# Performance work log

Measured on AMD Instinct MI355X. Metric: run time of the kernel, lower is better.

The kernel has to match this reference:

```python
import jax, jax.numpy as jnp
import numpy as np

V = 16384      # total nodes
G = 32         # nodes per graph (512 graphs)
D = 256        # node embedding dim == hidden_size
N = 8          # heads
H = 32         # head size
I = 1024       # intermediate size
LN_EPS = 1e-12


def _layer_norm(x, g, b):
    mu = jnp.mean(x, axis=-1, keepdims=True)
    var = jnp.mean(jnp.square(x - mu), axis=-1, keepdims=True)
    return (x - mu) * jax.lax.rsqrt(var + LN_EPS) * g + b


def setup_inputs() -> dict:
    key = jax.random.key(0)
    ks = jax.random.split(key, 5)
    node_embeddings = jax.random.normal(ks[0], (V, D), jnp.float32)
    # fully-connected pairs within each graph of size G (sorted by source node)
    idx = np.arange(V, dtype=np.int32).reshape(-1, G)          # [num_graphs, G]
    src = np.repeat(idx, G, axis=1).reshape(-1)                # [P]
    dst = np.tile(idx, (1, G)).reshape(-1)                     # [P]
    in_graph_node_pairs = jnp.asarray(np.stack([src, dst], axis=-1))  # [P, 2]
    s = 0.02
    return {
        "node_embeddings": node_embeddings,
        "in_graph_node_pairs": in_graph_node_pairs,
        "W_qkv": jax.random.normal(ks[1], (D, 3 * N * H), jnp.float32) * s,
        "W_o": jax.random.normal(ks[2], (N * H, D), jnp.float32) * s,
        "ln1_g": jnp.ones((D,), jnp.float32),
        "ln1_b": jnp.zeros((D,), jnp.float32),
        "W_i": jax.random.normal(ks[3], (D, I), jnp.float32) * s,
        "W_out2": jax.random.normal(ks[4], (I, D), jnp.float32) * s,
        "ln2_g": jnp.ones((D,), jnp.float32),
        "ln2_b": jnp.zeros((D,), jnp.float32),
    }


def reference(node_embeddings, in_graph_node_pairs, W_qkv, W_o, ln1_g, ln1_b,
              W_i, W_out2, ln2_g, ln2_b):
    nV = node_embeddings.shape[0]
    src = in_graph_node_pairs[:, 0]
    dst = in_graph_node_pairs[:, 1]
    # QKV projection -> [V, N, 3H] -> split
    qkv = (node_embeddings @ W_qkv).reshape(nV, N, 3 * H)
    q, k, v = jnp.split(qkv, 3, axis=-1)                       # each [V, N, H]
    # per-pair scores [P, N]
    scores = jnp.einsum('phi,phi->ph', q[src], k[dst]) / jnp.sqrt(jnp.float32(H))
    # segment softmax over source node, all heads at once
    m = jax.ops.segment_max(scores, src, num_segments=nV)       # [V, N]
    e = jnp.exp(scores - m[src])
    denom = jax.ops.segment_sum(e, src, num_segments=nV)        # [V, N]
    w = e / denom[src]                                          # [P, N]
    # weighted value scatter-sum -> [V, N, H]
    wv = w[:, :, None] * v[dst]
    att = jax.ops.segment_sum(wv, src, num_segments=nV).reshape(nV, N * H)
    # output projection + residual + LN
    pre = _layer_norm(att @ W_o + node_embeddings, ln1_g, ln1_b)
    inter = jax.nn.gelu(pre @ W_i, approximate=False)
    out = _layer_norm(inter @ W_out2 + pre, ln2_g, ln2_b)
    return out
```

## Files before the change

### kernel.cpp

```cpp
#include <hip/hip_runtime.h>
#include <math.h>

#define V 16384
#define D 256
#define NH 256
#define THREE_NH 768
#define IDIM 1024
#define LN_EPS 1e-12f
#define SCL 0.17677669529663687f

typedef short s16x8 __attribute__((ext_vector_type(8)));
typedef float f32x4 __attribute__((ext_vector_type(4)));

__device__ inline unsigned short f2bf(float f) {
    unsigned u = __float_as_uint(f);
    u += 0x7fffu + ((u >> 16) & 1u);
    return (unsigned short)(u >> 16);
}
__device__ inline float bf2f(unsigned short s) {
    return __uint_as_float(((unsigned)s) << 16);
}

__device__ inline float fast_erf(float x) {
    float ax = fabsf(x);
    float t  = 1.f / fmaf(0.3275911f, ax, 1.f);
    float p  = fmaf(fmaf(fmaf(fmaf(1.061405429f, t, -1.453152027f), t,
                              1.421413741f), t, -0.284496736f), t, 0.254829592f);
    float e  = 1.f - p * t * __expf(-ax * ax);
    return copysignf(e, x);
}

__device__ inline void gl2lds16(const unsigned short* g, unsigned short* l) {
    __builtin_amdgcn_global_load_lds(
        (__attribute__((address_space(1))) void*)(g),
        (__attribute__((address_space(3))) void*)(l), 16, 0, 0);
}

template <int ROWS_T>
__device__ inline void stage(const unsigned short* __restrict__ src, size_t row0,
                             int ldk, int k0, unsigned short* lds, int wv, int lane) {
    constexpr int PER_WAVE = ROWS_T / 32;
    #pragma unroll
    for (int i = 0; i < PER_WAVE; ++i) {
        const int seg = wv * PER_WAVE + i;
        const int r = seg * 8 + (lane >> 3);
        const int c = (lane & 7) ^ (r & 7);
        gl2lds16(src + (row0 + (size_t)r) * ldk + k0 + c * 8, lds + seg * 512);
    }
}

__device__ inline s16x8 fragld(const unsigned short* lds, int row, int chunk) {
    return *(const s16x8*)&lds[row * 64 + ((chunk ^ (row & 7)) << 3)];
}

__global__ __launch_bounds__(256) void prep(const float* __restrict__ X,
                                            unsigned short* __restrict__ Xb,
                                            const float* __restrict__ Wqkv,
                                            const float* __restrict__ Wo,
                                            const float* __restrict__ Wi,
                                            const float* __restrict__ Wo2,
                                            unsigned short* __restrict__ WqkvT,
                                            unsigned short* __restrict__ WoT,
                                            unsigned short* __restrict__ WiT,
                                            unsigned short* __restrict__ Wo2T) {
    const int b = blockIdx.x, t = threadIdx.x;
    if (b >= 768) {
        int i = (b - 768) * 256 + t;
        float4 v = ((const float4*)X)[i];
        ushort4 o;
        o.x = f2bf(v.x); o.y = f2bf(v.y); o.z = f2bf(v.z); o.w = f2bf(v.w);
        ((ushort4*)Xb)[i] = o;
        return;
    }
    __shared__ float tile[32][33];
    const float* W; unsigned short* Wt; int K, N, bx, by;
    if (b < 192)      { W = Wqkv; Wt = WqkvT; K = 256;  N = 768;  bx = b & 7;          by = b >> 3; }
    else if (b < 256) { W = Wo;   Wt = WoT;   K = 256;  N = 256;  bx = (b - 192) & 7;  by = (b - 192) >> 3; }
    else if (b < 512) { W = Wi;   Wt = WiT;   K = 256;  N = 1024; bx = (b - 256) & 7;  by = (b - 256) >> 3; }
    else              { W = Wo2;  Wt = Wo2T;  K = 1024; N = 256;  bx = (b - 512) & 31; by = (b - 512) >> 5; }
    const int k0 = bx * 32, n0 = by * 32;
    #pragma unroll
    for (int p = 0; p < 4; ++p) {
        int idx = t + p * 256, r = idx >> 5, c = idx & 31;
        tile[r][c] = W[(size_t)(k0 + r) * N + n0 + c];
    }
    __syncthreads();
    #pragma unroll
    for (int p = 0; p < 4; ++p) {
        int idx = t + p * 256, r = idx >> 5, c = idx & 31;
        Wt[(size_t)(n0 + r) * K + k0 + c] = f2bf(tile[c][r]);
    }
}

template <int K, int N, int EPI>
__global__ __launch_bounds__(256) void gemm128(const unsigned short* __restrict__ A,
                                               const unsigned short* __restrict__ Bt,
                                               unsigned short* __restrict__ C) {
    __shared__ unsigned short As[128 * 64];
    __shared__ unsigned short Bs[128 * 64];
    constexpr int NCOL = N / 128;
    const int b = blockIdx.x;
    const int idx = b >> 3;
    const int r0 = ((b & 7) * 16 + idx / NCOL) * 128;
    const int c0 = (idx % NCOL) * 128;
    const int t = threadIdx.x;
    const int wv = t >> 6, lane = t & 63, q = lane >> 4, l16 = lane & 15;
    const int wr = (wv >> 1) * 64, wc = (wv & 1) * 64;
    f32x4 acc[4][4] = {};

    for (int k0 = 0; k0 < K; k0 += 64) {
        __syncthreads();
        stage<128>(A,  (size_t)r0, K, k0, As, wv, lane);
        stage<128>(Bt, (size_t)c0, K, k0, Bs, wv, lane);
        __builtin_amdgcn_s_waitcnt(0);
        __syncthreads();
        #pragma unroll
        for (int kk2 = 0; kk2 < 2; ++kk2) {
            s16x8 af[4], bfr[4];
            #pragma unroll
            for (int mf = 0; mf < 4; ++mf)
                af[mf] = fragld(As, wr + mf * 16 + l16, kk2 * 4 + q);
            #pragma unroll
            for (int nf = 0; nf < 4; ++nf)
                bfr[nf] = fragld(Bs, wc + nf * 16 + l16, kk2 * 4 + q);
            #pragma unroll
            for (int mf = 0; mf < 4; ++mf)
                #pragma unroll
                for (int nf = 0; nf < 4; ++nf)
                    acc[mf][nf] = __builtin_amdgcn_mfma_f32_16x16x32_bf16(af[mf], bfr[nf], acc[mf][nf], 0, 0, 0);
        }
    }

    #pragma unroll
    for (int mf = 0; mf < 4; ++mf)
        #pragma unroll
        for (int nf = 0; nf < 4; ++nf) {
            const int cg = c0 + wc + nf * 16 + l16;
            #pragma unroll
            for (int r = 0; r < 4; ++r) {
                const int rg = r0 + wr + mf * 16 + q * 4 + r;
                float v = acc[mf][nf][r];
                if (EPI == 1) v = 0.5f * v * (1.f + fast_erf(v * 0.70710678118654752f));
                C[(size_t)rg * N + cg] = f2bf(v);
            }
        }
}

__global__ __launch_bounds__(256) void ffn_ln(const unsigned short* __restrict__ preb,
                                              const unsigned short* __restrict__ WiT,
                                              const unsigned short* __restrict__ Wo2T,
                                              const float* __restrict__ gamma,
                                              const float* __restrict__ beta,
                                              float* __restrict__ out) {
    __shared__ unsigned short Apre[32 * 64 * 4];
    __shared__ unsigned short Bs[256 * 64];
    __shared__ unsigned short Pbuf[32 * 64 * 4];
    __shared__ float2 partial[4][32];
    __shared__ float2 stats[32];
    const int t = threadIdx.x, r0 = blockIdx.x * 32;
    const int wv = t >> 6, lane = t & 63, q = lane >> 4, l16 = lane & 15;
    const int wc = wv * 64;
    f32x4 acc2[2][4] = {};

    #pragma unroll
    for (int kc = 0; kc < 4; ++kc)
        stage<32>(preb, (size_t)r0, 256, kc * 64, Apre + kc * 2048, wv, lane);

    for (int nc = 0; nc < 4; ++nc) {
        f32x4 acc1[2][4] = {};
        for (int k0 = 0; k0 < 256; k0 += 64) {
            __syncthreads();
            stage<256>(WiT, (size_t)nc * 256, 256, k0, Bs, wv, lane);
            __builtin_amdgcn_s_waitcnt(0);
            __syncthreads();
            const unsigned short* Ak = Apre + (k0 >> 6) * 2048;
            #pragma unroll
            for (int kk2 = 0; kk2 < 2; ++kk2) {
                s16x8 af[2], bfr[4];
                #pragma unroll
                for (int mf = 0; mf < 2; ++mf)
                    af[mf] = fragld(Ak, mf * 16 + l16, kk2 * 4 + q);
                #pragma unroll
                for (int nf = 0; nf < 4; ++nf)
                    bfr[nf] = fragld(Bs, wc + nf * 16 + l16, kk2 * 4 + q);
                #pragma unroll
                for (int mf = 0; mf < 2; ++mf)
                    #pragma unroll
                    for (int nf = 0; nf < 4; ++nf)
                        acc1[mf][nf] = __builtin_amdgcn_mfma_f32_16x16x32_bf16(af[mf], bfr[nf], acc1[mf][nf], 0, 0, 0);
            }
        }

        #pragma unroll
        for (int mf = 0; mf < 2; ++mf)
            #pragma unroll
            for (int nf = 0; nf < 4; ++nf)
                #pragma unroll
                for (int r = 0; r < 4; ++r) {
                    float v = acc1[mf][nf][r];
                    v = 0.5f * v * (1.f + fast_erf(v * 0.70710678118654752f));
                    const int i = mf * 16 + q * 4 + r;
                    const int colc = wc + nf * 16 + l16;
                    const int c8 = (colc >> 3) & 7;
                    Pbuf[wv * 2048 + i * 64 + ((c8 ^ (i & 7)) << 3) + (colc & 7)] = f2bf(v);
                }

        for (int ks = 0; ks < 256; ks += 64) {
            __syncthreads();
            stage<256>(Wo2T, 0, IDIM, nc * 256 + ks, Bs, wv, lane);
            __builtin_amdgcn_s_waitcnt(0);
            __syncthreads();
            const unsigned short* Pk = Pbuf + (ks >> 6) * 2048;
            #pragma unroll
            for (int kk2 = 0; kk2 < 2; ++kk2) {
                s16x8 af[2], bfr[4];
                #pragma unroll
                for (int mf = 0; mf < 2; ++mf)
                    af[mf] = fragld(Pk, mf * 16 + l16, kk2 * 4 + q);
                #pragma unroll
                for (int nf = 0; nf < 4; ++nf)
                    bfr[nf] = fragld(Bs, wc + nf * 16 + l16, kk2 * 4 + q);
                #pragma unroll
                for (int mf = 0; mf < 2; ++mf)
                    #pragma unroll
                    for (int nf = 0; nf < 4; ++nf)
                        acc2[mf][nf] = __builtin_amdgcn_mfma_f32_16x16x32_bf16(af[mf], bfr[nf], acc2[mf][nf], 0, 0, 0);
            }
        }
    }

    #pragma unroll
    for (int mf = 0; mf < 2; ++mf)
        #pragma unroll
        for (int nf = 0; nf < 4; ++nf) {
            const int cg = wc + nf * 16 + l16;
            const int kb = cg >> 6, c8 = (cg >> 3) & 7, e = cg & 7;
            #pragma unroll
            for (int r = 0; r < 4; ++r) {
                const int i = mf * 16 + q * 4 + r;
                acc2[mf][nf][r] += bf2f(Apre[kb * 2048 + i * 64 + ((c8 ^ (i & 7)) << 3) + e]);
            }
        }

    #pragma unroll
    for (int mf = 0; mf < 2; ++mf) {
        float s[4] = {0.f, 0.f, 0.f, 0.f}, ss[4] = {0.f, 0.f, 0.f, 0.f};
        #pragma unroll
        for (int nf = 0; nf < 4; ++nf)
            #pragma unroll
            for (int r = 0; r < 4; ++r) {
                float v = acc2[mf][nf][r];
                s[r] += v; ss[r] += v * v;
            }
        #pragma unroll
        for (int off = 1; off < 16; off <<= 1)
            #pragma unroll
            for (int r = 0; r < 4; ++r) {
                s[r]  += __shfl_xor(s[r],  off);
                ss[r] += __shfl_xor(ss[r], off);
            }
        if (l16 == 0)
            #pragma unroll
            for (int r = 0; r < 4; ++r)
                partial[wv][mf * 16 + q * 4 + r] = make_float2(s[r], ss[r]);
    }
    __syncthreads();
    if (t < 32) {
        float s = 0.f, ss = 0.f;
        #pragma unroll
        for (int w = 0; w < 4; ++w) { s += partial[w][t].x; ss += partial[w][t].y; }
        float mu  = s * (1.f / 256.f);
        float var = ss * (1.f / 256.f) - mu * mu;
        stats[t] = make_float2(mu, rsqrtf(var + LN_EPS));
    }
    __syncthreads();

    #pragma unroll
    for (int mf = 0; mf < 2; ++mf)
        #pragma unroll
        for (int nf = 0; nf < 4; ++nf) {
            const int cg = wc + nf * 16 + l16;
            const float g = gamma[cg], b = beta[cg];
            #pragma unroll
            for (int r = 0; r < 4; ++r) {
                const int rl = mf * 16 + q * 4 + r;
                const float2 st = stats[rl];
                out[(size_t)(r0 + rl) * NH + cg] = (acc2[mf][nf][r] - st.x) * st.y * g + b;
            }
        }
}

__global__ __launch_bounds__(256) void attln(const unsigned short* __restrict__ qkv,
                                             const unsigned short* __restrict__ WoT,
                                             const float* __restrict__ X,
                                             const float* __restrict__ gamma,
                                             const float* __restrict__ beta,
                                             unsigned short* __restrict__ preb) {
    __shared__ unsigned short smem[25216];
    unsigned short* Ks = smem;
    unsigned short* Vt = smem + 8192;
    unsigned short* Ps = smem + 16384;
    unsigned short* at = smem;
    unsigned short* Bs = smem + 8192;
    float2* partial = (float2*)(smem + 24576);
    float2* stats   = (float2*)(smem + 24576 + 512);

    const int g = blockIdx.x, t = threadIdx.x;
    const int wv = t >> 6, lane = t & 63, q = lane >> 4, l16 = lane & 15;
    const unsigned short* src = qkv + (size_t)g * 32 * THREE_NH;

    s16x8 qf[2][2];
    #pragma unroll
    for (int hh = 0; hh < 2; ++hh)
        #pragma unroll
        for (int mf = 0; mf < 2; ++mf)
            qf[hh][mf] = *(const s16x8*)&src[(size_t)(mf * 16 + l16) * THREE_NH +
                                             (wv * 2 + hh) * 96 + q * 8];

    s16x8 vld[4];
    int vh[4], vj[4], vdc[4];
    #pragma unroll
    for (int i = 0; i < 4; ++i) {
        int cid = i * 256 + t;
        vh[i] = cid >> 7; int rem = cid & 127; vj[i] = rem >> 2; vdc[i] = rem & 3;
        vld[i] = *(const s16x8*)&src[(size_t)vj[i] * THREE_NH + vh[i] * 96 + 64 + vdc[i] * 8];
    }

    #pragma unroll
    for (int i = 0; i < 4; ++i) {
        int ck = (wv * 4 + i) * 64 + lane;
        int h = ck >> 7, j = (ck >> 2) & 31, c = ck & 3;
        gl2lds16(src + (size_t)j * THREE_NH + h * 96 + 32 + c * 8, Ks + (wv * 4 + i) * 512);
    }

    #pragma unroll
    for (int i = 0; i < 4; ++i)
        #pragma unroll
        for (int e = 0; e < 8; ++e) {
            int d = vdc[i] * 8 + e;
            Vt[vh[i] * 1024 + d * 32 + ((((vj[i] >> 3) ^ ((d >> 2) & 3))) << 3) + (vj[i] & 7)] =
                (unsigned short)vld[i][e];
        }

    __builtin_amdgcn_s_waitcnt(0);
    __syncthreads();

    f32x4 sacc[2][2][2] = {};
    #pragma unroll
    for (int hh = 0; hh < 2; ++hh) {
        const int h = wv * 2 + hh;
        #pragma unroll
        for (int nf = 0; nf < 2; ++nf) {
            s16x8 kf = *(const s16x8*)&Ks[h * 1024 + (nf * 16 + l16) * 32 + q * 8];
            #pragma unroll
            for (int mf = 0; mf < 2; ++mf)
                sacc[hh][mf][nf] = __builtin_amdgcn_mfma_f32_16x16x32_bf16(
                    qf[hh][mf], kf, sacc[hh][mf][nf], 0, 0, 0);
        }
    }

    float inv[2][2][4];
    #pragma unroll
    for (int hh = 0; hh < 2; ++hh) {
        const int h = wv * 2 + hh;
        #pragma unroll
        for (int mf = 0; mf < 2; ++mf)
            #pragma unroll
            for (int r = 0; r < 4; ++r) {
                float a0 = sacc[hh][mf][0][r], a1 = sacc[hh][mf][1][r];
                float m = fmaxf(a0, a1);
                m = fmaxf(m, __shfl_xor(m, 1));
                m = fmaxf(m, __shfl_xor(m, 2));
                m = fmaxf(m, __shfl_xor(m, 4));
                m = fmaxf(m, __shfl_xor(m, 8));
                float e0 = __expf((a0 - m) * SCL);
                float e1 = __expf((a1 - m) * SCL);
                float sm = e0 + e1;
                sm += __shfl_xor(sm, 1);
                sm += __shfl_xor(sm, 2);
                sm += __shfl_xor(sm, 4);
                sm += __shfl_xor(sm, 8);
                inv[hh][mf][r] = 1.f / sm;
                const int row = mf * 16 + q * 4 + r;
                const int base = h * 1024 + row * 32 + (l16 & 7);
                Ps[base + ((((l16 >> 3) ^ q)) << 3)]       = f2bf(e0);
                Ps[base + ((((2 + (l16 >> 3)) ^ q)) << 3)] = f2bf(e1);
            }
    }

    f32x4 oacc[2][2][2] = {};
    #pragma unroll
    for (int hh = 0; hh < 2; ++hh) {
        const int h = wv * 2 + hh;
        const int sw = (l16 >> 2) & 3;
        s16x8 pa[2], vb[2];
        #pragma unroll
        for (int mf = 0; mf < 2; ++mf)
            pa[mf] = *(const s16x8*)&Ps[h * 1024 + (mf * 16 + l16) * 32 + ((q ^ sw) << 3)];
        #pragma unroll
        for (int nf = 0; nf < 2; ++nf)
            vb[nf] = *(const s16x8*)&Vt[h * 1024 + (nf * 16 + l16) * 32 + ((q ^ sw) << 3)];
        #pragma unroll
        for (int mf = 0; mf < 2; ++mf)
            #pragma unroll
            for (int nf = 0; nf < 2; ++nf)
                oacc[hh][mf][nf] = __builtin_amdgcn_mfma_f32_16x16x32_bf16(
                    pa[mf], vb[nf], oacc[hh][mf][nf], 0, 0, 0);
    }
    __syncthreads();

    #pragma unroll
    for (int hh = 0; hh < 2; ++hh)
        #pragma unroll
        for (int mf = 0; mf < 2; ++mf)
            #pragma unroll
            for (int nf = 0; nf < 2; ++nf)
                #pragma unroll
                for (int r = 0; r < 4; ++r) {
                    float val = oacc[hh][mf][nf][r] * inv[hh][mf][r];
                    const int i = mf * 16 + q * 4 + r;
                    const int col = (wv * 2 + hh) * 32 + nf * 16 + l16;
                    const int kb = col >> 6, c = (col >> 3) & 7;
                    at[kb * 2048 + i * 64 + ((c ^ (i & 7)) << 3) + (col & 7)] = f2bf(val);
                }

    const int wc = wv * 64;
    const int r0 = g * 32;
    f32x4 acc[2][4] = {};

    for (int k0 = 0; k0 < 256; k0 += 64) {
        __syncthreads();
        stage<256>(WoT, 0, 256, k0, Bs, wv, lane);
        __builtin_amdgcn_s_waitcnt(0);
        __syncthreads();
        const unsigned short* atk = at + (k0 >> 6) * 2048;
        #pragma unroll
        for (int kk2 = 0; kk2 < 2; ++kk2) {
            s16x8 af[2], bfr[4];
            #pragma unroll
            for (int mf = 0; mf < 2; ++mf)
                af[mf] = fragld(atk, mf * 16 + l16, kk2 * 4 + q);
            #pragma unroll
            for (int nf = 0; nf < 4; ++nf)
                bfr[nf] = fragld(Bs, wc + nf * 16 + l16, kk2 * 4 + q);
            #pragma unroll
            for (int mf = 0; mf < 2; ++mf)
                #pragma unroll
                for (int nf = 0; nf < 4; ++nf)
                    acc[mf][nf] = __builtin_amdgcn_mfma_f32_16x16x32_bf16(af[mf], bfr[nf], acc[mf][nf], 0, 0, 0);
        }
    }

    #pragma unroll
    for (int mf = 0; mf < 2; ++mf)
        #pragma unroll
        for (int nf = 0; nf < 4; ++nf) {
            const int cg = wc + nf * 16 + l16;
            #pragma unroll
            for (int r = 0; r < 4; ++r)
                acc[mf][nf][r] += X[(size_t)(r0 + mf * 16 + q * 4 + r) * NH + cg];
        }

    #pragma unroll
    for (int mf = 0; mf < 2; ++mf) {
        float sp[4] = {0.f, 0.f, 0.f, 0.f}, ssp[4] = {0.f, 0.f, 0.f, 0.f};
        #pragma unroll
        for (int nf = 0; nf < 4; ++nf)
            #pragma unroll
            for (int r = 0; r < 4; ++r) {
                float v = acc[mf][nf][r];
                sp[r] += v; ssp[r] += v * v;
            }
        #pragma unroll
        for (int off = 1; off < 16; off <<= 1)
            #pragma unroll
            for (int r = 0; r < 4; ++r) {
                sp[r]  += __shfl_xor(sp[r],  off);
                ssp[r] += __shfl_xor(ssp[r], off);
            }
        if (l16 == 0)
            #pragma unroll
            for (int r = 0; r < 4; ++r)
                partial[wv * 32 + mf * 16 + q * 4 + r] = make_float2(sp[r], ssp[r]);
    }
    __syncthreads();
    if (t < 32) {
        float sv = 0.f, ssv = 0.f;
        #pragma unroll
        for (int w = 0; w < 4; ++w) { sv += partial[w * 32 + t].x; ssv += partial[w * 32 + t].y; }
        float mu  = sv * (1.f / 256.f);
        float var = ssv * (1.f / 256.f) - mu * mu;
        stats[t] = make_float2(mu, rsqrtf(var + LN_EPS));
    }
    __syncthreads();

    #pragma unroll
    for (int mf = 0; mf < 2; ++mf)
        #pragma unroll
        for (int nf = 0; nf < 4; ++nf) {
            const int cg = wc + nf * 16 + l16;
            const float gm = gamma[cg], bt = beta[cg];
            #pragma unroll
            for (int r = 0; r < 4; ++r) {
                const int rl = mf * 16 + q * 4 + r;
                const float2 st = stats[rl];
                float v = (acc[mf][nf][r] - st.x) * st.y * gm + bt;
                preb[(size_t)(r0 + rl) * NH + cg] = f2bf(v);
            }
        }
}

extern "C" void kernel_launch(void* const* d_in, const int* in_sizes, int n_in,
                              void* d_out, int out_size, void* d_ws, size_t ws_size,
                              hipStream_t stream) {
    const float* X      = (const float*)d_in[0];
    const float* W_qkv  = (const float*)d_in[2];
    const float* W_o    = (const float*)d_in[3];
    const float* ln1_g  = (const float*)d_in[4];
    const float* ln1_b  = (const float*)d_in[5];
    const float* W_i    = (const float*)d_in[6];
    const float* W_out2 = (const float*)d_in[7];
    const float* ln2_g  = (const float*)d_in[8];
    const float* ln2_b  = (const float*)d_in[9];
    float* out = (float*)d_out;

    char* ws = (char*)d_ws;
    unsigned short* Xbf   = (unsigned short*)(ws);
    unsigned short* qkvb  = (unsigned short*)(ws + 8388608);
    unsigned short* preb  = (unsigned short*)(ws + 58720256);
    unsigned short* WqkvT = (unsigned short*)(ws + 67108864);
    unsigned short* WoT   = (unsigned short*)(ws + 67502080);
    unsigned short* WiT   = (unsigned short*)(ws + 67633152);
    unsigned short* Wo2T  = (unsigned short*)(ws + 68157440);

    dim3 blk(256);
    hipLaunchKernelGGL(prep, dim3(768 + V * D / 4 / 256), blk, 0, stream,
                       X, Xbf, W_qkv, W_o, W_i, W_out2, WqkvT, WoT, WiT, Wo2T);

    hipLaunchKernelGGL((gemm128<D, THREE_NH, 0>), dim3(V / 128 * (THREE_NH / 128)), blk, 0, stream,
                       Xbf, WqkvT, qkvb);
    hipLaunchKernelGGL(attln, dim3(V / 32), blk, 0, stream,
                       qkvb, WoT, X, ln1_g, ln1_b, preb);
    hipLaunchKernelGGL(ffn_ln, dim3(V / 32), blk, 0, stream,
                       preb, WiT, Wo2T, ln2_g, ln2_b, out);
}
```

Baseline: 158.1 us.

## Load weight fragments directly from global memory instead of staging through LDS

In the FFN and attention-output GEMMs, each wave now reads its B-operand (weight) fragments straight from global memory into registers instead of cooperatively staging tiles into shared memory. This drops the weight staging buffer and most of the per-k-step barriers and waitcnt stalls, and frees LDS, which may allow higher occupancy. The cost is that each wave reads its own weight columns without sharing across waves, so performance relies on L1/L2 caching of the small weight matrices and on loads issued earlier in the unrolled loops hiding latency.

```diff
diff --git a/kernel.cpp b/kernel.cpp
--- a/kernel.cpp
+++ b/kernel.cpp
@@ -153,7 +153,6 @@
                                               const float* __restrict__ beta,
                                               float* __restrict__ out) {
     __shared__ unsigned short Apre[32 * 64 * 4];
-    __shared__ unsigned short Bs[256 * 64];
     __shared__ unsigned short Pbuf[32 * 64 * 4];
     __shared__ float2 partial[4][32];
     __shared__ float2 stats[32];
@@ -165,29 +164,31 @@
     #pragma unroll
     for (int kc = 0; kc < 4; ++kc)
         stage<32>(preb, (size_t)r0, 256, kc * 64, Apre + kc * 2048, wv, lane);
+    __builtin_amdgcn_s_waitcnt(0);
+    __syncthreads();
+
+    const unsigned short* Bp2 = Wo2T + (size_t)(wc + l16) * IDIM;
 
     for (int nc = 0; nc < 4; ++nc) {
+        const unsigned short* Bp1 = WiT + (size_t)(nc * 256 + wc + l16) * 256;
         f32x4 acc1[2][4] = {};
+        #pragma unroll
         for (int k0 = 0; k0 < 256; k0 += 64) {
-            __syncthreads();
-            stage<256>(WiT, (size_t)nc * 256, 256, k0, Bs, wv, lane);
-            __builtin_amdgcn_s_waitcnt(0);
-            __syncthreads();
             const unsigned short* Ak = Apre + (k0 >> 6) * 2048;
             #pragma unroll
             for (int kk2 = 0; kk2 < 2; ++kk2) {
-                s16x8 af[2], bfr[4];
+                s16x8 af[2], bv[4];
                 #pragma unroll
                 for (int mf = 0; mf < 2; ++mf)
                     af[mf] = fragld(Ak, mf * 16 + l16, kk2 * 4 + q);
                 #pragma unroll
                 for (int nf = 0; nf < 4; ++nf)
-                    bfr[nf] = fragld(Bs, wc + nf * 16 + l16, kk2 * 4 + q);
+                    bv[nf] = *(const s16x8*)&Bp1[(size_t)nf * 16 * 256 + k0 + (kk2 * 4 + q) * 8];
                 #pragma unroll
                 for (int mf = 0; mf < 2; ++mf)
                     #pragma unroll
                     for (int nf = 0; nf < 4; ++nf)
-                        acc1[mf][nf] = __builtin_amdgcn_mfma_f32_16x16x32_bf16(af[mf], bfr[nf], acc1[mf][nf], 0, 0, 0);
+                        acc1[mf][nf] = __builtin_amdgcn_mfma_f32_16x16x32_bf16(af[mf], bv[nf], acc1[mf][nf], 0, 0, 0);
             }
         }
 
@@ -204,29 +205,28 @@
                     const int c8 = (colc >> 3) & 7;
                     Pbuf[wv * 2048 + i * 64 + ((c8 ^ (i & 7)) << 3) + (colc & 7)] = f2bf(v);
                 }
-
+        __syncthreads();
+
+        #pragma unroll
         for (int ks = 0; ks < 256; ks += 64) {
-            __syncthreads();
-            stage<256>(Wo2T, 0, IDIM, nc * 256 + ks, Bs, wv, lane);
-            __builtin_amdgcn_s_waitcnt(0);
-            __syncthreads();
             const unsigned short* Pk = Pbuf + (ks >> 6) * 2048;
             #pragma unroll
             for (int kk2 = 0; kk2 < 2; ++kk2) {
-                s16x8 af[2], bfr[4];
+                s16x8 af[2], bv[4];
                 #pragma unroll
                 for (int mf = 0; mf < 2; ++mf)
                     af[mf] = fragld(Pk, mf * 16 + l16, kk2 * 4 + q);
                 #pragma unroll
                 for (int nf = 0; nf < 4; ++nf)
-                    bfr[nf] = fragld(Bs, wc + nf * 16 + l16, kk2 * 4 + q);
+                    bv[nf] = *(const s16x8*)&Bp2[(size_t)nf * 16 * IDIM + nc * 256 + ks + (kk2 * 4 + q) * 8];
                 #pragma unroll
                 for (int mf = 0; mf < 2; ++mf)
                     #pragma unroll
                     for (int nf = 0; nf < 4; ++nf)
-                        acc2[mf][nf] = __builtin_amdgcn_mfma_f32_16x16x32_bf16(af[mf], bfr[nf], acc2[mf][nf], 0, 0, 0);
-            }
-        }
+                        acc2[mf][nf] = __builtin_amdgcn_mfma_f32_16x16x32_bf16(af[mf], bv[nf], acc2[mf][nf], 0, 0, 0);
+            }
+        }
+        __syncthreads();
     }
 
     #pragma unroll
@@ -301,7 +301,6 @@
     unsigned short* Vt = smem + 8192;
     unsigned short* Ps = smem + 16384;
     unsigned short* at = smem;
-    unsigned short* Bs = smem + 8192;
     float2* partial = (float2*)(smem + 24576);
     float2* stats   = (float2*)(smem + 24576 + 512);
 
@@ -423,31 +422,30 @@
                     const int kb = col >> 6, c = (col >> 3) & 7;
                     at[kb * 2048 + i * 64 + ((c ^ (i & 7)) << 3) + (col & 7)] = f2bf(val);
                 }
+    __syncthreads();
 
     const int wc = wv * 64;
     const int r0 = g * 32;
     f32x4 acc[2][4] = {};
-
-    for (int k0 = 0; k0 < 256; k0 += 64) {
-        __syncthreads();
-        stage<256>(WoT, 0, 256, k0, Bs, wv, lane);
-        __builtin_amdgcn_s_waitcnt(0);
-        __syncthreads();
-        const unsigned short* atk = at + (k0 >> 6) * 2048;
+    const unsigned short* Bp = WoT + (size_t)(wc + l16) * NH;
+
+    #pragma unroll
+    for (int kc = 0; kc < 4; ++kc) {
+        const unsigned short* atk = at + kc * 2048;
         #pragma unroll
         for (int kk2 = 0; kk2 < 2; ++kk2) {
-            s16x8 af[2], bfr[4];
+            s16x8 af[2], bv[4];
             #pragma unroll
             for (int mf = 0; mf < 2; ++mf)
                 af[mf] = fragld(atk, mf * 16 + l16, kk2 * 4 + q);
             #pragma unroll
             for (int nf = 0; nf < 4; ++nf)
-                bfr[nf] = fragld(Bs, wc + nf * 16 + l16, kk2 * 4 + q);
+                bv[nf] = *(const s16x8*)&Bp[(size_t)nf * 16 * NH + kc * 64 + (kk2 * 4 + q) * 8];
             #pragma unroll
             for (int mf = 0; mf < 2; ++mf)
                 #pragma unroll
                 for (int nf = 0; nf < 4; ++nf)
-                    acc[mf][nf] = __builtin_amdgcn_mfma_f32_16x16x32_bf16(af[mf], bfr[nf], acc[mf][nf], 0, 0, 0);
+                    acc[mf][nf] = __builtin_amdgcn_mfma_f32_16x16x32_bf16(af[mf], bv[nf], acc[mf][nf], 0, 0, 0);
         }
     }
 
```

Measured after the change: 185.6 us. +17.4%, slower.
